# Kernel tuning notes

Measured on AMD Instinct MI355X. Metric: run time of the kernel, lower is better.

## Reference

```python
import jax, jax.numpy as jnp
import numpy as np

N_NODES = 50000
N_EDGES = 800000
N_FEAT = 128
HIDDEN = 64
N_LAYERS = 3
N_GRAPHS = 512
N_CLASSES = 10
BN_EPS = 1e-5


def setup_inputs() -> dict:
    key = jax.random.key(0)
    ks = jax.random.split(key, 16)
    s = 1.0 / np.sqrt(HIDDEN)
    inp = {
        "x": jax.random.normal(ks[0], (N_NODES, N_FEAT), dtype=jnp.float32),
        "edge_index": jax.random.randint(ks[1], (2, N_EDGES), 0, N_NODES, dtype=jnp.int32),
        "batch": jnp.sort(jax.random.randint(ks[2], (N_NODES,), 0, N_GRAPHS, dtype=jnp.int32)),
        "enc_w": jax.random.normal(ks[3], (N_FEAT, HIDDEN), dtype=jnp.float32) / np.sqrt(N_FEAT),
        "enc_b": jnp.zeros((HIDDEN,), dtype=jnp.float32),
        "eps": jnp.zeros((N_LAYERS,), dtype=jnp.float32),
        "conv_w1": jax.random.normal(ks[4], (N_LAYERS, HIDDEN, HIDDEN), dtype=jnp.float32) * s,
        "conv_b1": jnp.zeros((N_LAYERS, HIDDEN), dtype=jnp.float32),
        "conv_w2": jax.random.normal(ks[5], (N_LAYERS, HIDDEN, HIDDEN), dtype=jnp.float32) * s,
        "conv_b2": jnp.zeros((N_LAYERS, HIDDEN), dtype=jnp.float32),
        "bn_gamma": jnp.ones((N_LAYERS, HIDDEN), dtype=jnp.float32),
        "bn_beta": jnp.zeros((N_LAYERS, HIDDEN), dtype=jnp.float32),
        "lin_w": jax.random.normal(ks[6], (HIDDEN, N_CLASSES), dtype=jnp.float32) * s,
        "lin_b": jnp.zeros((N_CLASSES,), dtype=jnp.float32),
    }
    return inp


def reference(x, edge_index, batch, enc_w, enc_b, eps, conv_w1, conv_b1,
              conv_w2, conv_b2, bn_gamma, bn_beta, lin_w, lin_b):
    n = x.shape[0]
    src, dst = edge_index[0], edge_index[1]
    h = x @ enc_w + enc_b  # [N, H] encoder
    for l in range(N_LAYERS):
        # GINConv: sum-aggregate neighbor features, add (1+eps)*self, 2-layer MLP
        agg = jax.ops.segment_sum(h[src], dst, num_segments=n)
        z = (1.0 + eps[l]) * h + agg
        z = jnp.maximum(z @ conv_w1[l] + conv_b1[l], 0.0) @ conv_w2[l] + conv_b2[l]
        # BatchNorm1d (batch statistics) + ReLU; dropout omitted (eval mode)
        mean = jnp.mean(z, axis=0)
        var = jnp.mean(jnp.square(z - mean), axis=0)
        z = (z - mean) * jax.lax.rsqrt(var + BN_EPS) * bn_gamma[l] + bn_beta[l]
        h = jnp.maximum(z, 0.0)
    # global mean pool over graphs
    pooled = jax.ops.segment_sum(h, batch, num_segments=N_GRAPHS)
    counts = jax.ops.segment_sum(jnp.ones((n,), dtype=h.dtype), batch, num_segments=N_GRAPHS)
    pooled = pooled / jnp.maximum(counts, 1.0)[:, None]
    return pooled @ lin_w + lin_b  # [N_GRAPHS, N_CLASSES]
```

## Files before the change

kernel.cpp:

```cpp
#include <hip/hip_runtime.h>

#define N_NODES   50000
#define N_EDGES   800000
#define N_FEAT    128
#define HIDDEN    64
#define N_LAYERS  3
#define N_GRAPHS  512
#define N_CLASSES 10
#define BN_EPS    1e-5f
#define SCAN_BLK  196
#define LWAVES    8

__device__ __forceinline__ int swz(int c, int g) { return g ^ (c & 15); }

__global__ __launch_bounds__(512, 6) void enc_kernel(
    const float* __restrict__ x, const float* __restrict__ w,
    const float* __restrict__ b, float* __restrict__ h)
{
    __shared__ __align__(16) float wT[HIDDEN * N_FEAT];
    __shared__ __align__(16) float xb[LWAVES][4][N_FEAT];
    for (int i = threadIdx.x; i < N_FEAT * HIDDEN; i += 512) {
        int k = i >> 6, c = i & 63;
        wT[c * 128 + swz(c, k >> 2) * 4 + (k & 3)] = w[i];
    }
    const int lane = threadIdx.x & 63;
    const int wv   = threadIdx.x >> 6;
    const int sz   = lane & 15;
    const int r2   = lane >> 5;
    const int cc   = (lane & 31) * 4;
    const float bias = b[lane];
    __syncthreads();
    const int nwaves = gridDim.x * LWAVES;
    for (int grp = blockIdx.x * LWAVES + wv; grp < N_NODES / 4; grp += nwaves) {
        const int nbase = grp * 4;
        float4 v0 = *(const float4*)&x[(size_t)(nbase + r2) * N_FEAT + cc];
        float4 v1 = *(const float4*)&x[(size_t)(nbase + 2 + r2) * N_FEAT + cc];
        *((float4*)&xb[wv][r2][cc])     = v0;
        *((float4*)&xb[wv][2 + r2][cc]) = v1;
        float o0 = bias, o1 = bias, o2 = bias, o3 = bias;
        #pragma unroll 8
        for (int kc = 0; kc < N_FEAT / 4; ++kc) {
            float4 w4 = *(const float4*)&wT[lane * 128 + ((kc ^ sz) << 2)];
            float4 z0 = *(const float4*)&xb[wv][0][4 * kc];
            float4 z1 = *(const float4*)&xb[wv][1][4 * kc];
            float4 z2 = *(const float4*)&xb[wv][2][4 * kc];
            float4 z3 = *(const float4*)&xb[wv][3][4 * kc];
            o0 = fmaf(w4.x, z0.x, fmaf(w4.y, z0.y, fmaf(w4.z, z0.z, fmaf(w4.w, z0.w, o0))));
            o1 = fmaf(w4.x, z1.x, fmaf(w4.y, z1.y, fmaf(w4.z, z1.z, fmaf(w4.w, z1.w, o1))));
            o2 = fmaf(w4.x, z2.x, fmaf(w4.y, z2.y, fmaf(w4.z, z2.z, fmaf(w4.w, z2.w, o2))));
            o3 = fmaf(w4.x, z3.x, fmaf(w4.y, z3.y, fmaf(w4.z, z3.z, fmaf(w4.w, z3.w, o3))));
        }
        h[(size_t)(nbase + 0) * HIDDEN + lane] = o0;
        h[(size_t)(nbase + 1) * HIDDEN + lane] = o1;
        h[(size_t)(nbase + 2) * HIDDEN + lane] = o2;
        h[(size_t)(nbase + 3) * HIDDEN + lane] = o3;
    }
}

__global__ __launch_bounds__(256) void hist_kernel(const int* __restrict__ ei,
                                                   int* __restrict__ deg)
{
    int e = blockIdx.x * 256 + threadIdx.x;
    if (e < N_EDGES) atomicAdd(&deg[ei[N_EDGES + e]], 1);
}

__global__ __launch_bounds__(256) void scan1_kernel(const int* __restrict__ deg,
                                                    int* __restrict__ row_start,
                                                    int* __restrict__ bsum)
{
    __shared__ int s[256];
    const int tid = threadIdx.x;
    const int gid = blockIdx.x * 256 + tid;
    int v = (gid < N_NODES) ? deg[gid] : 0;
    s[tid] = v;
    __syncthreads();
    for (int off = 1; off < 256; off <<= 1) {
        int t = (tid >= off) ? s[tid - off] : 0;
        __syncthreads();
        if (tid >= off) s[tid] += t;
        __syncthreads();
    }
    if (gid < N_NODES) row_start[gid] = s[tid] - v;
    if (tid == 255) bsum[blockIdx.x] = s[255];
}

__global__ __launch_bounds__(256) void scan2_kernel(int* __restrict__ bsum,
                                                    int* __restrict__ row_start)
{
    __shared__ int s[256];
    const int tid = threadIdx.x;
    int v = (tid < SCAN_BLK) ? bsum[tid] : 0;
    s[tid] = v;
    __syncthreads();
    for (int off = 1; off < 256; off <<= 1) {
        int t = (tid >= off) ? s[tid - off] : 0;
        __syncthreads();
        if (tid >= off) s[tid] += t;
        __syncthreads();
    }
    if (tid < SCAN_BLK) bsum[tid] = s[tid] - v;
    if (tid == 255) row_start[N_NODES] = s[255];
}

__global__ __launch_bounds__(256) void scan3_kernel(int* __restrict__ row_start,
                                                    const int* __restrict__ bsum,
                                                    int* __restrict__ cursor)
{
    int gid = blockIdx.x * 256 + threadIdx.x;
    if (gid < N_NODES) {
        int v = row_start[gid] + bsum[blockIdx.x];
        row_start[gid] = v;
        cursor[gid] = v;
    }
}

__global__ __launch_bounds__(256) void fill_kernel(const int* __restrict__ ei,
                                                   int* __restrict__ cursor,
                                                   int* __restrict__ csr_src)
{
    int e = blockIdx.x * 256 + threadIdx.x;
    if (e >= N_EDGES) return;
    int d = ei[N_EDGES + e];
    int pos = atomicAdd(&cursor[d], 1);
    csr_src[pos] = ei[e];
}

template<bool HASBN>
__global__ __launch_bounds__(512, 8) void layer_kernel(
    const float* __restrict__ hin, const int* __restrict__ csr_src,
    const int* __restrict__ row_start,
    const float* __restrict__ stats_prev, const float* __restrict__ gamma,
    const float* __restrict__ beta,
    const float* __restrict__ eps, int layer,
    const float* __restrict__ w1, const float* __restrict__ b1,
    const float* __restrict__ w2, const float* __restrict__ b2,
    float* __restrict__ hout, float* __restrict__ stats_cur)
{
    __shared__ __align__(16) float wT1[HIDDEN * HIDDEN];
    __shared__ __align__(16) float wT2[HIDDEN * HIDDEN];
    __shared__ __align__(16) float zb[LWAVES][4][HIDDEN];
    for (int i = threadIdx.x; i < HIDDEN * HIDDEN; i += 512) {
        int k = i >> 6, c = i & 63;
        int dst = c * 64 + swz(c, k >> 2) * 4 + (k & 3);
        wT1[dst] = w1[i];
        wT2[dst] = w2[i];
    }
    const int lane = threadIdx.x & 63;
    const int wv   = threadIdx.x >> 6;
    const int q    = lane >> 4;
    const int c4   = (lane & 15) * 4;
    const int sz   = lane & 15;
    float Ag[4] = {1.f, 1.f, 1.f, 1.f}, Bg[4] = {0.f, 0.f, 0.f, 0.f};
    if (HASBN) {
        const float invN = 1.0f / (float)N_NODES;
        #pragma unroll
        for (int t = 0; t < 4; ++t) {
            float mean = stats_prev[c4 + t] * invN;
            float var  = stats_prev[HIDDEN + c4 + t] * invN - mean * mean;
            float inv  = rsqrtf(fmaxf(var, 0.f) + BN_EPS);
            Ag[t] = inv * gamma[c4 + t];
            Bg[t] = beta[c4 + t] - mean * Ag[t];
        }
    }
    const float sf  = 1.0f + eps[layer];
    const float b1c = b1[lane], b2c = b2[lane];
    __syncthreads();

    float s = 0.f, s2 = 0.f;
    const int nwaves = gridDim.x * LWAVES;
    for (int grp = blockIdx.x * LWAVES + wv; grp < N_NODES / 4; grp += nwaves) {
        const int nbase = grp * 4;
        #pragma unroll
        for (int n = 0; n < 4; ++n) {
            const int node = nbase + n;
            const int s0 = row_start[node];
            const int s1 = row_start[node + 1];
            float a0 = 0.f, a1 = 0.f, a2 = 0.f, a3 = 0.f;
            for (int jb = s0; jb < s1; jb += 64) {
                int m = s1 - jb; if (m > 64) m = 64;
                int idx = csr_src[jb + (lane < m ? lane : m - 1)];
                int mm = m & ~3;
                for (int j = 0; j < mm; j += 4) {
                    int i = __shfl(idx, j + q);
                    const float* r = &hin[(size_t)i * HIDDEN + c4];
                    float4 u = *(const float4*)r;
                    if (HASBN) {
                        u.x = fmaxf(fmaf(u.x, Ag[0], Bg[0]), 0.f);
                        u.y = fmaxf(fmaf(u.y, Ag[1], Bg[1]), 0.f);
                        u.z = fmaxf(fmaf(u.z, Ag[2], Bg[2]), 0.f);
                        u.w = fmaxf(fmaf(u.w, Ag[3], Bg[3]), 0.f);
                    }
                    a0 += u.x; a1 += u.y; a2 += u.z; a3 += u.w;
                }
                int r3 = m & 3;
                if (r3) {
                    int sl = mm + q;
                    int i = __shfl(idx, sl < m ? sl : m - 1);
                    const float* r = &hin[(size_t)i * HIDDEN + c4];
                    float4 u = *(const float4*)r;
                    if (HASBN) {
                        u.x = fmaxf(fmaf(u.x, Ag[0], Bg[0]), 0.f);
                        u.y = fmaxf(fmaf(u.y, Ag[1], Bg[1]), 0.f);
                        u.z = fmaxf(fmaf(u.z, Ag[2], Bg[2]), 0.f);
                        u.w = fmaxf(fmaf(u.w, Ag[3], Bg[3]), 0.f);
                    }
                    if (q < r3) { a0 += u.x; a1 += u.y; a2 += u.z; a3 += u.w; }
                }
            }
            a0 += __shfl_xor(a0, 16); a1 += __shfl_xor(a1, 16);
            a2 += __shfl_xor(a2, 16); a3 += __shfl_xor(a3, 16);
            a0 += __shfl_xor(a0, 32); a1 += __shfl_xor(a1, 32);
            a2 += __shfl_xor(a2, 32); a3 += __shfl_xor(a3, 32);
            float4 sv = *(const float4*)&hin[(size_t)node * HIDDEN + c4];
            if (HASBN) {
                sv.x = fmaxf(fmaf(sv.x, Ag[0], Bg[0]), 0.f);
                sv.y = fmaxf(fmaf(sv.y, Ag[1], Bg[1]), 0.f);
                sv.z = fmaxf(fmaf(sv.z, Ag[2], Bg[2]), 0.f);
                sv.w = fmaxf(fmaf(sv.w, Ag[3], Bg[3]), 0.f);
            }
            if (q == 0) {
                float4 z4;
                z4.x = fmaf(sf, sv.x, a0);
                z4.y = fmaf(sf, sv.y, a1);
                z4.z = fmaf(sf, sv.z, a2);
                z4.w = fmaf(sf, sv.w, a3);
                *((float4*)&zb[wv][n][c4]) = z4;
            }
        }
        float o0 = b1c, o1 = b1c, o2 = b1c, o3 = b1c;
        #pragma unroll 4
        for (int kc = 0; kc < HIDDEN / 4; ++kc) {
            float4 w4 = *(const float4*)&wT1[lane * 64 + ((kc ^ sz) << 2)];
            float4 z0 = *(const float4*)&zb[wv][0][4 * kc];
            float4 z1 = *(const float4*)&zb[wv][1][4 * kc];
            float4 z2 = *(const float4*)&zb[wv][2][4 * kc];
            float4 z3 = *(const float4*)&zb[wv][3][4 * kc];
            o0 = fmaf(w4.x, z0.x, fmaf(w4.y, z0.y, fmaf(w4.z, z0.z, fmaf(w4.w, z0.w, o0))));
            o1 = fmaf(w4.x, z1.x, fmaf(w4.y, z1.y, fmaf(w4.z, z1.z, fmaf(w4.w, z1.w, o1))));
            o2 = fmaf(w4.x, z2.x, fmaf(w4.y, z2.y, fmaf(w4.z, z2.z, fmaf(w4.w, z2.w, o2))));
            o3 = fmaf(w4.x, z3.x, fmaf(w4.y, z3.y, fmaf(w4.z, z3.z, fmaf(w4.w, z3.w, o3))));
        }
        zb[wv][0][lane] = fmaxf(o0, 0.f);
        zb[wv][1][lane] = fmaxf(o1, 0.f);
        zb[wv][2][lane] = fmaxf(o2, 0.f);
        zb[wv][3][lane] = fmaxf(o3, 0.f);
        float p0 = b2c, p1 = b2c, p2 = b2c, p3 = b2c;
        #pragma unroll 4
        for (int kc = 0; kc < HIDDEN / 4; ++kc) {
            float4 w4 = *(const float4*)&wT2[lane * 64 + ((kc ^ sz) << 2)];
            float4 z0 = *(const float4*)&zb[wv][0][4 * kc];
            float4 z1 = *(const float4*)&zb[wv][1][4 * kc];
            float4 z2 = *(const float4*)&zb[wv][2][4 * kc];
            float4 z3 = *(const float4*)&zb[wv][3][4 * kc];
            p0 = fmaf(w4.x, z0.x, fmaf(w4.y, z0.y, fmaf(w4.z, z0.z, fmaf(w4.w, z0.w, p0))));
            p1 = fmaf(w4.x, z1.x, fmaf(w4.y, z1.y, fmaf(w4.z, z1.z, fmaf(w4.w, z1.w, p1))));
            p2 = fmaf(w4.x, z2.x, fmaf(w4.y, z2.y, fmaf(w4.z, z2.z, fmaf(w4.w, z2.w, p2))));
            p3 = fmaf(w4.x, z3.x, fmaf(w4.y, z3.y, fmaf(w4.z, z3.z, fmaf(w4.w, z3.w, p3))));
        }
        hout[(size_t)(nbase + 0) * HIDDEN + lane] = p0;
        hout[(size_t)(nbase + 1) * HIDDEN + lane] = p1;
        hout[(size_t)(nbase + 2) * HIDDEN + lane] = p2;
        hout[(size_t)(nbase + 3) * HIDDEN + lane] = p3;
        s  += ((p0 + p1) + (p2 + p3));
        s2 += ((p0 * p0 + p1 * p1) + (p2 * p2 + p3 * p3));
    }
    __syncthreads();
    float* red = &zb[0][0][0];
    red[threadIdx.x] = s;
    red[512 + threadIdx.x] = s2;
    __syncthreads();
    if (wv == 0) {
        float ts = 0.f, ts2 = 0.f;
        #pragma unroll
        for (int wq = 0; wq < LWAVES; ++wq) {
            ts  += red[wq * 64 + lane];
            ts2 += red[512 + wq * 64 + lane];
        }
        atomicAdd(&stats_cur[lane], ts);
        atomicAdd(&stats_cur[HIDDEN + lane], ts2);
    }
}

__device__ __forceinline__ int lbound(const int* __restrict__ a, int n, int v)
{
    int lo = 0, hi = n;
    while (lo < hi) { int m = (lo + hi) >> 1; if (a[m] < v) lo = m + 1; else hi = m; }
    return lo;
}

__global__ __launch_bounds__(256) void pool_kernel(
    const float* __restrict__ hpre, const int* __restrict__ batch,
    const float* __restrict__ stats, const float* __restrict__ gamma,
    const float* __restrict__ beta, float* __restrict__ pooled)
{
    __shared__ int bounds[2];
    __shared__ float red[256];
    const int g = blockIdx.x;
    if (threadIdx.x < 2)
        bounds[threadIdx.x] = lbound(batch, N_NODES, g + threadIdx.x);
    __syncthreads();
    const int start = bounds[0], end = bounds[1];
    const int col = threadIdx.x & 63;
    const int row = threadIdx.x >> 6;
    const float invN = 1.0f / (float)N_NODES;
    float mean = stats[col] * invN;
    float var  = stats[HIDDEN + col] * invN - mean * mean;
    float inv  = rsqrtf(fmaxf(var, 0.f) + BN_EPS);
    float A = inv * gamma[col];
    float B = beta[col] - mean * A;
    float s = 0.f;
    for (int r = start + row; r < end; r += 4)
        s += fmaxf(fmaf(hpre[(size_t)r * HIDDEN + col], A, B), 0.f);
    red[threadIdx.x] = s;
    __syncthreads();
    if (row == 0) {
        float t = red[col] + red[64 + col] + red[128 + col] + red[192 + col];
        pooled[(size_t)g * HIDDEN + col] = t / fmaxf((float)(end - start), 1.0f);
    }
}

__global__ void out_kernel(const float* __restrict__ pooled,
                           const float* __restrict__ w, const float* __restrict__ b,
                           float* __restrict__ out)
{
    int gid = blockIdx.x * blockDim.x + threadIdx.x;
    if (gid >= N_GRAPHS * N_CLASSES) return;
    int g = gid / N_CLASSES;
    int c = gid - g * N_CLASSES;
    float acc = b[c];
    for (int j = 0; j < HIDDEN; ++j)
        acc = fmaf(pooled[(size_t)g * HIDDEN + j], w[j * N_CLASSES + c], acc);
    out[gid] = acc;
}

extern "C" void kernel_launch(void* const* d_in, const int* in_sizes, int n_in,
                              void* d_out, int out_size, void* d_ws, size_t ws_size,
                              hipStream_t stream)
{
    const float* x       = (const float*)d_in[0];
    const int*   ei      = (const int*)d_in[1];
    const int*   batch   = (const int*)d_in[2];
    const float* enc_w   = (const float*)d_in[3];
    const float* enc_b   = (const float*)d_in[4];
    const float* eps     = (const float*)d_in[5];
    const float* conv_w1 = (const float*)d_in[6];
    const float* conv_b1 = (const float*)d_in[7];
    const float* conv_w2 = (const float*)d_in[8];
    const float* conv_b2 = (const float*)d_in[9];
    const float* bn_g    = (const float*)d_in[10];
    const float* bn_b    = (const float*)d_in[11];
    const float* lin_w   = (const float*)d_in[12];
    const float* lin_b   = (const float*)d_in[13];
    float* out = (float*)d_out;

    char* ws = (char*)d_ws;
    const size_t HB = (size_t)N_NODES * HIDDEN * sizeof(float);
    size_t off = 0;
    float* P      = (float*)(ws + off); off += HB;
    float* Q      = (float*)(ws + off); off += HB;
    float* stats  = (float*)(ws + off); off += N_LAYERS * 2 * HIDDEN * sizeof(float);
    float* pooled = (float*)(ws + off); off += (size_t)N_GRAPHS * HIDDEN * sizeof(float);
    int* deg       = (int*)(ws + off); off += 50176 * sizeof(int);
    int* row_start = (int*)(ws + off); off += 50176 * sizeof(int);
    int* cursor    = (int*)(ws + off); off += 50176 * sizeof(int);
    int* bsum      = (int*)(ws + off); off += 256 * sizeof(int);
    int* csr_src   = (int*)(ws + off); off += (size_t)N_EDGES * sizeof(int);

    hipMemsetAsync(deg, 0, N_NODES * sizeof(int), stream);
    hipMemsetAsync(stats, 0, N_LAYERS * 2 * HIDDEN * sizeof(float), stream);

    enc_kernel<<<768, 512, 0, stream>>>(x, enc_w, enc_b, P);

    hist_kernel<<<(N_EDGES + 255) / 256, 256, 0, stream>>>(ei, deg);
    scan1_kernel<<<SCAN_BLK, 256, 0, stream>>>(deg, row_start, bsum);
    scan2_kernel<<<1, 256, 0, stream>>>(bsum, row_start);
    scan3_kernel<<<SCAN_BLK, 256, 0, stream>>>(row_start, bsum, cursor);
    fill_kernel<<<(N_EDGES + 255) / 256, 256, 0, stream>>>(ei, cursor, csr_src);

    const float* curin = P;
    float* curout = Q;
    for (int l = 0; l < N_LAYERS; ++l) {
        const float* w1 = conv_w1 + (size_t)l * HIDDEN * HIDDEN;
        const float* b1 = conv_b1 + (size_t)l * HIDDEN;
        const float* w2 = conv_w2 + (size_t)l * HIDDEN * HIDDEN;
        const float* b2 = conv_b2 + (size_t)l * HIDDEN;
        if (l == 0)
            layer_kernel<false><<<1024, 512, 0, stream>>>(
                curin, csr_src, row_start, nullptr, nullptr, nullptr,
                eps, l, w1, b1, w2, b2, curout, stats);
        else
            layer_kernel<true><<<1024, 512, 0, stream>>>(
                curin, csr_src, row_start,
                stats + (size_t)(l - 1) * 2 * HIDDEN,
                bn_g + (size_t)(l - 1) * HIDDEN, bn_b + (size_t)(l - 1) * HIDDEN,
                eps, l, w1, b1, w2, b2, curout, stats + (size_t)l * 2 * HIDDEN);
        const float* t = curout; curout = (float*)curin; curin = t;
    }

    pool_kernel<<<N_GRAPHS, 256, 0, stream>>>(
        Q, batch, stats + (size_t)(N_LAYERS - 1) * 2 * HIDDEN,
        bn_g + (size_t)(N_LAYERS - 1) * HIDDEN, bn_b + (size_t)(N_LAYERS - 1) * HIDDEN,
        pooled);
    out_kernel<<<(N_GRAPHS * N_CLASSES + 255) / 256, 256, 0, stream>>>(pooled, lin_w, lin_b, out);
}
```

Measured before the change: 339.1 us.

## Store hidden activations as bf16 and aggregate with fixed-point integer sums

Hidden states between layers are stored as packed bf16 pairs, halving gather traffic in the neighbor aggregation, which now has each lane read 8 features per edge. Aggregation accumulates in 16.16 fixed-point integers, making the sum order-independent. BN statistics atomics are replaced by per-block partials plus a small reduce kernel, and the deg memset is folded into the encoder. bf16 storage and fixed-point quantization lower accuracy and could exceed tolerance.

```diff
diff --git a/kernel.cpp b/kernel.cpp
--- a/kernel.cpp
+++ b/kernel.cpp
@@ -10,15 +10,37 @@
 #define BN_EPS    1e-5f
 #define SCAN_BLK  196
 #define LWAVES    8
+#define HP        32
+#define NBLK      1024
+#define QSCALE    65536.0f
+#define QINV      (1.0f / 65536.0f)
 
 __device__ __forceinline__ int swz(int c, int g) { return g ^ (c & 15); }
+
+__device__ __forceinline__ unsigned bf16rne(float x)
+{
+    unsigned u = __float_as_uint(x);
+    return (u + 0x7fffu + ((u >> 16) & 1u)) >> 16;
+}
+__device__ __forceinline__ float2 bf2(unsigned u)
+{
+    float2 r;
+    r.x = __uint_as_float(u << 16);
+    r.y = __uint_as_float(u & 0xffff0000u);
+    return r;
+}
 
 __global__ __launch_bounds__(512, 6) void enc_kernel(
     const float* __restrict__ x, const float* __restrict__ w,
-    const float* __restrict__ b, float* __restrict__ h)
+    const float* __restrict__ b, unsigned* __restrict__ h,
+    int* __restrict__ deg)
 {
     __shared__ __align__(16) float wT[HIDDEN * N_FEAT];
     __shared__ __align__(16) float xb[LWAVES][4][N_FEAT];
+    {
+        int g = blockIdx.x * 512 + threadIdx.x;
+        if (g < N_NODES) deg[g] = 0;
+    }
     for (int i = threadIdx.x; i < N_FEAT * HIDDEN; i += 512) {
         int k = i >> 6, c = i & 63;
         wT[c * 128 + swz(c, k >> 2) * 4 + (k & 3)] = w[i];
@@ -50,10 +72,15 @@
             o2 = fmaf(w4.x, z2.x, fmaf(w4.y, z2.y, fmaf(w4.z, z2.z, fmaf(w4.w, z2.w, o2))));
             o3 = fmaf(w4.x, z3.x, fmaf(w4.y, z3.y, fmaf(w4.z, z3.z, fmaf(w4.w, z3.w, o3))));
         }
-        h[(size_t)(nbase + 0) * HIDDEN + lane] = o0;
-        h[(size_t)(nbase + 1) * HIDDEN + lane] = o1;
-        h[(size_t)(nbase + 2) * HIDDEN + lane] = o2;
-        h[(size_t)(nbase + 3) * HIDDEN + lane] = o3;
+        float t0 = __shfl_xor(o0, 1), t1 = __shfl_xor(o1, 1);
+        float t2 = __shfl_xor(o2, 1), t3 = __shfl_xor(o3, 1);
+        if (!(lane & 1)) {
+            int p = lane >> 1;
+            h[(size_t)(nbase + 0) * HP + p] = bf16rne(o0) | (bf16rne(t0) << 16);
+            h[(size_t)(nbase + 1) * HP + p] = bf16rne(o1) | (bf16rne(t1) << 16);
+            h[(size_t)(nbase + 2) * HP + p] = bf16rne(o2) | (bf16rne(t2) << 16);
+            h[(size_t)(nbase + 3) * HP + p] = bf16rne(o3) | (bf16rne(t3) << 16);
+        }
     }
 }
 
@@ -127,14 +154,14 @@
 
 template<bool HASBN>
 __global__ __launch_bounds__(512, 8) void layer_kernel(
-    const float* __restrict__ hin, const int* __restrict__ csr_src,
+    const unsigned* __restrict__ hin, const int* __restrict__ csr_src,
     const int* __restrict__ row_start,
     const float* __restrict__ stats_prev, const float* __restrict__ gamma,
     const float* __restrict__ beta,
     const float* __restrict__ eps, int layer,
     const float* __restrict__ w1, const float* __restrict__ b1,
     const float* __restrict__ w2, const float* __restrict__ b2,
-    float* __restrict__ hout, float* __restrict__ stats_cur)
+    unsigned* __restrict__ hout, float* __restrict__ partials)
 {
     __shared__ __align__(16) float wT1[HIDDEN * HIDDEN];
     __shared__ __align__(16) float wT2[HIDDEN * HIDDEN];
@@ -147,19 +174,22 @@
     }
     const int lane = threadIdx.x & 63;
     const int wv   = threadIdx.x >> 6;
-    const int q    = lane >> 4;
-    const int c4   = (lane & 15) * 4;
+    const int o    = lane >> 3;
+    const int c8   = (lane & 7) * 4;
+    const int cb   = c8 * 2;
     const int sz   = lane & 15;
-    float Ag[4] = {1.f, 1.f, 1.f, 1.f}, Bg[4] = {0.f, 0.f, 0.f, 0.f};
+    float Ag[8], Bg[8];
+    #pragma unroll
+    for (int t = 0; t < 8; ++t) { Ag[t] = 1.f; Bg[t] = 0.f; }
     if (HASBN) {
         const float invN = 1.0f / (float)N_NODES;
         #pragma unroll
-        for (int t = 0; t < 4; ++t) {
-            float mean = stats_prev[c4 + t] * invN;
-            float var  = stats_prev[HIDDEN + c4 + t] * invN - mean * mean;
+        for (int t = 0; t < 8; ++t) {
+            float mean = stats_prev[cb + t] * invN;
+            float var  = stats_prev[HIDDEN + cb + t] * invN - mean * mean;
             float inv  = rsqrtf(fmaxf(var, 0.f) + BN_EPS);
-            Ag[t] = inv * gamma[c4 + t];
-            Bg[t] = beta[c4 + t] - mean * Ag[t];
+            Ag[t] = inv * gamma[cb + t];
+            Bg[t] = beta[cb + t] - mean * Ag[t];
         }
     }
     const float sf  = 1.0f + eps[layer];
@@ -175,56 +205,63 @@
             const int node = nbase + n;
             const int s0 = row_start[node];
             const int s1 = row_start[node + 1];
-            float a0 = 0.f, a1 = 0.f, a2 = 0.f, a3 = 0.f;
+            int a[8];
+            #pragma unroll
+            for (int t = 0; t < 8; ++t) a[t] = 0;
             for (int jb = s0; jb < s1; jb += 64) {
                 int m = s1 - jb; if (m > 64) m = 64;
                 int idx = csr_src[jb + (lane < m ? lane : m - 1)];
-                int mm = m & ~3;
-                for (int j = 0; j < mm; j += 4) {
-                    int i = __shfl(idx, j + q);
-                    const float* r = &hin[(size_t)i * HIDDEN + c4];
-                    float4 u = *(const float4*)r;
-                    if (HASBN) {
-                        u.x = fmaxf(fmaf(u.x, Ag[0], Bg[0]), 0.f);
-                        u.y = fmaxf(fmaf(u.y, Ag[1], Bg[1]), 0.f);
-                        u.z = fmaxf(fmaf(u.z, Ag[2], Bg[2]), 0.f);
-                        u.w = fmaxf(fmaf(u.w, Ag[3], Bg[3]), 0.f);
+                int mm = m & ~7;
+                for (int j = 0; j < mm; j += 8) {
+                    int i = __shfl(idx, j + o);
+                    uint4 u = *(const uint4*)&hin[(size_t)i * HP + c8];
+                    float2 f0 = bf2(u.x), f1 = bf2(u.y), f2 = bf2(u.z), f3 = bf2(u.w);
+                    float v[8] = {f0.x, f0.y, f1.x, f1.y, f2.x, f2.y, f3.x, f3.y};
+                    #pragma unroll
+                    for (int t = 0; t < 8; ++t) {
+                        float f = v[t];
+                        if (HASBN) f = fmaxf(fmaf(f, Ag[t], Bg[t]), 0.f);
+                        a[t] += (int)(f * QSCALE);
                     }
-                    a0 += u.x; a1 += u.y; a2 += u.z; a3 += u.w;
                 }
-                int r3 = m & 3;
-                if (r3) {
-                    int sl = mm + q;
+                int r8 = m & 7;
+                if (r8) {
+                    int sl = mm + o;
                     int i = __shfl(idx, sl < m ? sl : m - 1);
-                    const float* r = &hin[(size_t)i * HIDDEN + c4];
-                    float4 u = *(const float4*)r;
-                    if (HASBN) {
-                        u.x = fmaxf(fmaf(u.x, Ag[0], Bg[0]), 0.f);
-                        u.y = fmaxf(fmaf(u.y, Ag[1], Bg[1]), 0.f);
-                        u.z = fmaxf(fmaf(u.z, Ag[2], Bg[2]), 0.f);
-                        u.w = fmaxf(fmaf(u.w, Ag[3], Bg[3]), 0.f);
+                    if (o < r8) {
+                        uint4 u = *(const uint4*)&hin[(size_t)i * HP + c8];
+                        float2 f0 = bf2(u.x), f1 = bf2(u.y), f2 = bf2(u.z), f3 = bf2(u.w);
+                        float v[8] = {f0.x, f0.y, f1.x, f1.y, f2.x, f2.y, f3.x, f3.y};
+                        #pragma unroll
+                        for (int t = 0; t < 8; ++t) {
+                            float f = v[t];
+                            if (HASBN) f = fmaxf(fmaf(f, Ag[t], Bg[t]), 0.f);
+                            a[t] += (int)(f * QSCALE);
+                        }
                     }
-                    if (q < r3) { a0 += u.x; a1 += u.y; a2 += u.z; a3 += u.w; }
                 }
             }
-            a0 += __shfl_xor(a0, 16); a1 += __shfl_xor(a1, 16);
-            a2 += __shfl_xor(a2, 16); a3 += __shfl_xor(a3, 16);
-            a0 += __shfl_xor(a0, 32); a1 += __shfl_xor(a1, 32);
-            a2 += __shfl_xor(a2, 32); a3 += __shfl_xor(a3, 32);
-            float4 sv = *(const float4*)&hin[(size_t)node * HIDDEN + c4];
-            if (HASBN) {
-                sv.x = fmaxf(fmaf(sv.x, Ag[0], Bg[0]), 0.f);
-                sv.y = fmaxf(fmaf(sv.y, Ag[1], Bg[1]), 0.f);
-                sv.z = fmaxf(fmaf(sv.z, Ag[2], Bg[2]), 0.f);
-                sv.w = fmaxf(fmaf(sv.w, Ag[3], Bg[3]), 0.f);
+            #pragma unroll
+            for (int t = 0; t < 8; ++t) {
+                a[t] += __shfl_xor(a[t], 8);
+                a[t] += __shfl_xor(a[t], 16);
+                a[t] += __shfl_xor(a[t], 32);
             }
-            if (q == 0) {
-                float4 z4;
-                z4.x = fmaf(sf, sv.x, a0);
-                z4.y = fmaf(sf, sv.y, a1);
-                z4.z = fmaf(sf, sv.z, a2);
-                z4.w = fmaf(sf, sv.w, a3);
-                *((float4*)&zb[wv][n][c4]) = z4;
+            if (o == 0) {
+                uint4 su = *(const uint4*)&hin[(size_t)node * HP + c8];
+                float2 g0 = bf2(su.x), g1 = bf2(su.y), g2 = bf2(su.z), g3 = bf2(su.w);
+                float svv[8] = {g0.x, g0.y, g1.x, g1.y, g2.x, g2.y, g3.x, g3.y};
+                float zo[8];
+                #pragma unroll
+                for (int t = 0; t < 8; ++t) {
+                    float f = svv[t];
+                    if (HASBN) f = fmaxf(fmaf(f, Ag[t], Bg[t]), 0.f);
+                    zo[t] = fmaf(sf, f, (float)a[t] * QINV);
+                }
+                float4 q0 = {zo[0], zo[1], zo[2], zo[3]};
+                float4 q1 = {zo[4], zo[5], zo[6], zo[7]};
+                *((float4*)&zb[wv][n][cb])     = q0;
+                *((float4*)&zb[wv][n][cb + 4]) = q1;
             }
         }
         float o0 = b1c, o1 = b1c, o2 = b1c, o3 = b1c;
@@ -257,10 +294,15 @@
             p2 = fmaf(w4.x, z2.x, fmaf(w4.y, z2.y, fmaf(w4.z, z2.z, fmaf(w4.w, z2.w, p2))));
             p3 = fmaf(w4.x, z3.x, fmaf(w4.y, z3.y, fmaf(w4.z, z3.z, fmaf(w4.w, z3.w, p3))));
         }
-        hout[(size_t)(nbase + 0) * HIDDEN + lane] = p0;
-        hout[(size_t)(nbase + 1) * HIDDEN + lane] = p1;
-        hout[(size_t)(nbase + 2) * HIDDEN + lane] = p2;
-        hout[(size_t)(nbase + 3) * HIDDEN + lane] = p3;
+        float t0 = __shfl_xor(p0, 1), t1 = __shfl_xor(p1, 1);
+        float t2 = __shfl_xor(p2, 1), t3 = __shfl_xor(p3, 1);
+        if (!(lane & 1)) {
+            int p = lane >> 1;
+            hout[(size_t)(nbase + 0) * HP + p] = bf16rne(p0) | (bf16rne(t0) << 16);
+            hout[(size_t)(nbase + 1) * HP + p] = bf16rne(p1) | (bf16rne(t1) << 16);
+            hout[(size_t)(nbase + 2) * HP + p] = bf16rne(p2) | (bf16rne(t2) << 16);
+            hout[(size_t)(nbase + 3) * HP + p] = bf16rne(p3) | (bf16rne(t3) << 16);
+        }
         s  += ((p0 + p1) + (p2 + p3));
         s2 += ((p0 * p0 + p1 * p1) + (p2 * p2 + p3 * p3));
     }
@@ -276,8 +318,28 @@
             ts  += red[wq * 64 + lane];
             ts2 += red[512 + wq * 64 + lane];
         }
-        atomicAdd(&stats_cur[lane], ts);
-        atomicAdd(&stats_cur[HIDDEN + lane], ts2);
+        partials[(size_t)blockIdx.x * 128 + lane]      = ts;
+        partials[(size_t)blockIdx.x * 128 + 64 + lane] = ts2;
+    }
+}
+
+__global__ __launch_bounds__(1024) void stats_reduce_kernel(
+    const float* __restrict__ partials, float* __restrict__ stats)
+{
+    __shared__ float red[8][128];
+    const int c = threadIdx.x & 127;
+    const int k = threadIdx.x >> 7;
+    float s = 0.f;
+    #pragma unroll 4
+    for (int b = k * 128; b < (k + 1) * 128; ++b)
+        s += partials[(size_t)b * 128 + c];
+    red[k][c] = s;
+    __syncthreads();
+    if (k == 0) {
+        float t = 0.f;
+        #pragma unroll
+        for (int kk = 0; kk < 8; ++kk) t += red[kk][c];
+        stats[c] = t;
     }
 }
 
@@ -289,7 +351,7 @@
 }
 
 __global__ __launch_bounds__(256) void pool_kernel(
-    const float* __restrict__ hpre, const int* __restrict__ batch,
+    const unsigned* __restrict__ hpre, const int* __restrict__ batch,
     const float* __restrict__ stats, const float* __restrict__ gamma,
     const float* __restrict__ beta, float* __restrict__ pooled)
 {
@@ -309,8 +371,12 @@
     float A = inv * gamma[col];
     float B = beta[col] - mean * A;
     float s = 0.f;
-    for (int r = start + row; r < end; r += 4)
-        s += fmaxf(fmaf(hpre[(size_t)r * HIDDEN + col], A, B), 0.f);
+    for (int r = start + row; r < end; r += 4) {
+        unsigned u = hpre[(size_t)r * HP + (col >> 1)];
+        float v = (col & 1) ? __uint_as_float(u & 0xffff0000u)
+                            : __uint_as_float(u << 16);
+        s += fmaxf(fmaf(v, A, B), 0.f);
+    }
     red[threadIdx.x] = s;
     __syncthreads();
     if (row == 0) {
@@ -354,22 +420,20 @@
     float* out = (float*)d_out;
 
     char* ws = (char*)d_ws;
-    const size_t HB = (size_t)N_NODES * HIDDEN * sizeof(float);
+    const size_t HB = (size_t)N_NODES * HP * sizeof(unsigned);
     size_t off = 0;
-    float* P      = (float*)(ws + off); off += HB;
-    float* Q      = (float*)(ws + off); off += HB;
-    float* stats  = (float*)(ws + off); off += N_LAYERS * 2 * HIDDEN * sizeof(float);
-    float* pooled = (float*)(ws + off); off += (size_t)N_GRAPHS * HIDDEN * sizeof(float);
+    unsigned* P    = (unsigned*)(ws + off); off += HB;
+    unsigned* Q    = (unsigned*)(ws + off); off += HB;
+    float* stats   = (float*)(ws + off); off += N_LAYERS * 2 * HIDDEN * sizeof(float);
+    float* pooled  = (float*)(ws + off); off += (size_t)N_GRAPHS * HIDDEN * sizeof(float);
+    float* partials= (float*)(ws + off); off += (size_t)NBLK * 128 * sizeof(float);
     int* deg       = (int*)(ws + off); off += 50176 * sizeof(int);
     int* row_start = (int*)(ws + off); off += 50176 * sizeof(int);
     int* cursor    = (int*)(ws + off); off += 50176 * sizeof(int);
     int* bsum      = (int*)(ws + off); off += 256 * sizeof(int);
     int* csr_src   = (int*)(ws + off); off += (size_t)N_EDGES * sizeof(int);
 
-    hipMemsetAsync(deg, 0, N_NODES * sizeof(int), stream);
-    hipMemsetAsync(stats, 0, N_LAYERS * 2 * HIDDEN * sizeof(float), stream);
-
-    enc_kernel<<<768, 512, 0, stream>>>(x, enc_w, enc_b, P);
+    enc_kernel<<<768, 512, 0, stream>>>(x, enc_w, enc_b, P, deg);
 
     hist_kernel<<<(N_EDGES + 255) / 256, 256, 0, stream>>>(ei, deg);
     scan1_kernel<<<SCAN_BLK, 256, 0, stream>>>(deg, row_start, bsum);
@@ -377,24 +441,26 @@
     scan3_kernel<<<SCAN_BLK, 256, 0, stream>>>(row_start, bsum, cursor);
     fill_kernel<<<(N_EDGES + 255) / 256, 256, 0, stream>>>(ei, cursor, csr_src);
 
-    const float* curin = P;
-    float* curout = Q;
+    const unsigned* curin = P;
+    unsigned* curout = Q;
     for (int l = 0; l < N_LAYERS; ++l) {
         const float* w1 = conv_w1 + (size_t)l * HIDDEN * HIDDEN;
         const float* b1 = conv_b1 + (size_t)l * HIDDEN;
         const float* w2 = conv_w2 + (size_t)l * HIDDEN * HIDDEN;
         const float* b2 = conv_b2 + (size_t)l * HIDDEN;
         if (l == 0)
-            layer_kernel<false><<<1024, 512, 0, stream>>>(
+            layer_kernel<false><<<NBLK, 512, 0, stream>>>(
                 curin, csr_src, row_start, nullptr, nullptr, nullptr,
-                eps, l, w1, b1, w2, b2, curout, stats);
+                eps, l, w1, b1, w2, b2, curout, partials);
         else
-            layer_kernel<true><<<1024, 512, 0, stream>>>(
+            layer_kernel<true><<<NBLK, 512, 0, stream>>>(
                 curin, csr_src, row_start,
                 stats + (size_t)(l - 1) * 2 * HIDDEN,
                 bn_g + (size_t)(l - 1) * HIDDEN, bn_b + (size_t)(l - 1) * HIDDEN,
-                eps, l, w1, b1, w2, b2, curout, stats + (size_t)l * 2 * HIDDEN);
-        const float* t = curout; curout = (float*)curin; curin = t;
+                eps, l, w1, b1, w2, b2, curout, partials);
+        stats_reduce_kernel<<<1, 1024, 0, stream>>>(partials,
+                                                    stats + (size_t)l * 2 * HIDDEN);
+        const unsigned* t = curout; curout = (unsigned*)curin; curin = t;
     }
 
     pool_kernel<<<N_GRAPHS, 256, 0, stream>>>(
```

New measurement: 332.6 us. About the same (-1.9%).
